# Kernel tuning notes

Measured on AMD Instinct MI355X. Metric: run time of the kernel, lower is better.

## Reference

```python
import jax, jax.numpy as jnp
import numpy as np

D_MODEL = 256
NUM_HEADS = 8
DEPTH = D_MODEL // NUM_HEADS
NEG_BIG = -1e9


def setup_inputs() -> dict:
    key = jax.random.key(0)
    ks = jax.random.split(key, 8)
    B, S = 4, 2048
    inp = {
        "v": jax.random.normal(ks[0], (B, S, D_MODEL), dtype=jnp.float32),
        "k": jax.random.normal(ks[1], (B, S, D_MODEL), dtype=jnp.float32),
        "q": jax.random.normal(ks[2], (B, S, D_MODEL), dtype=jnp.float32),
        "mask": jnp.ones((B, S), dtype=jnp.float32),
        # kernel_size-1 Conv1D without bias == dense projection (d_in, d_out)
        "Wq": jax.random.normal(ks[3], (D_MODEL, D_MODEL), dtype=jnp.float32) * 0.05,
        "Wk": jax.random.normal(ks[4], (D_MODEL, D_MODEL), dtype=jnp.float32) * 0.05,
        "Wv": jax.random.normal(ks[5], (D_MODEL, D_MODEL), dtype=jnp.float32) * 0.05,
        "Wo": jax.random.normal(ks[6], (D_MODEL, D_MODEL), dtype=jnp.float32) * 0.05,
    }
    return inp


def _split_heads(x):
    # (B, S, d_model) -> (B, H, S, depth)
    B, S, _ = x.shape
    return x.reshape(B, S, NUM_HEADS, DEPTH).transpose(0, 2, 1, 3)


def reference(v, k, q, mask, Wq, Wk, Wv, Wo):
    B, S, _ = q.shape
    qh = _split_heads(q @ Wq)  # (B,H,Sq,depth)
    kh = _split_heads(k @ Wk)  # (B,H,Sk,depth)
    vh = _split_heads(v @ Wv)  # (B,H,Sk,depth)

    scale = 1.0 / jnp.sqrt(jnp.asarray(DEPTH, dtype=jnp.float32))
    logits = jnp.einsum("bhqd,bhkd->bhqk", qh, kh) * scale  # (B,H,Sq,Sk)
    mask_att = mask[:, None, None, :]  # broadcast over heads and query dim
    logits = logits + (1.0 - mask_att) * NEG_BIG
    attn = jax.nn.softmax(logits, axis=-1)  # (B,H,Sq,Sk)

    ctx = jnp.einsum("bhqk,bhkd->bhqd", attn, vh)  # (B,H,Sq,depth)
    concat = ctx.transpose(0, 2, 1, 3).reshape(B, S, D_MODEL)
    out = concat @ Wo
    return (out, attn)
```

## Files before the change

### kernel.cpp

```cpp
#include <hip/hip_runtime.h>

#define BB 4
#define HH 8
#define SS 2048
#define DD 32
#define DMODEL 256
#define NEG_BIG_F (-1000000000.0f)
#define SCALE 0.17677669529663687f
#define L2E 1.4426950408889634f
#define SC2 (SCALE * L2E)

typedef short short8 __attribute__((ext_vector_type(8)));
typedef float float4_ __attribute__((ext_vector_type(4)));

__device__ __forceinline__ unsigned short f2bf(float x) {
  unsigned u = __float_as_uint(x);
  u += 0x7FFFu + ((u >> 16) & 1u);
  return (unsigned short)(u >> 16);
}

__device__ __forceinline__ unsigned cvtpk(float lo, float hi) {
  unsigned u;
  asm("v_cvt_pk_bf16_f32 %0, %1, %2" : "=v"(u) : "v"(lo), "v"(hi));
  return u;
}

__global__ __launch_bounds__(256) void prep_w(
    const float* __restrict__ Wq, const float* __restrict__ Wk,
    const float* __restrict__ Wv, const float* __restrict__ Wo,
    unsigned short* __restrict__ wt) {
  __shared__ float tile[32][33];
  int z = blockIdx.z;
  const float* W = (z == 0) ? Wq : (z == 1) ? Wk : (z == 2) ? Wv : Wo;
  unsigned short* dst = wt + (size_t)z * DMODEL * DMODEL;
  int k0 = blockIdx.x * 32, n0 = blockIdx.y * 32;
  int tx = threadIdx.x & 31, ty = threadIdx.x >> 5;
  for (int r = ty; r < 32; r += 8)
    tile[r][tx] = W[(size_t)(k0 + r) * DMODEL + n0 + tx];
  __syncthreads();
  for (int r = ty; r < 32; r += 8)
    dst[(size_t)(n0 + r) * DMODEL + k0 + tx] = f2bf(tile[tx][r]);
}

__global__ __launch_bounds__(256) void proj_kernel(
    const float* __restrict__ q, const float* __restrict__ k,
    const float* __restrict__ v, const unsigned short* __restrict__ wt,
    unsigned short* __restrict__ qh, unsigned short* __restrict__ kh,
    unsigned short* __restrict__ vT) {
  int z = blockIdx.z;
  const float* src = (z == 0) ? q : (z == 1) ? k : v;
  const unsigned short* Wt = wt + (size_t)z * DMODEL * DMODEL;

  int w = threadIdx.x >> 6, lane = threadIdx.x & 63, l16 = lane & 15,
      g = lane >> 4;
  int row = blockIdx.x * 64 + w * 16 + l16;
  int n0 = blockIdx.y * 64;

  float4_ z4 = {0.f, 0.f, 0.f, 0.f};
  float4_ acc[4] = {z4, z4, z4, z4};

  for (int k0 = 0; k0 < DMODEL; k0 += 32) {
    const float4_* ap = (const float4_*)(src + (size_t)row * DMODEL + k0 + 8 * g);
    float4_ a0 = ap[0], a1 = ap[1];
    short8 a;
#pragma unroll
    for (int j = 0; j < 4; ++j) {
      a[j] = (short)f2bf(a0[j]);
      a[4 + j] = (short)f2bf(a1[j]);
    }
#pragma unroll
    for (int cb = 0; cb < 4; ++cb) {
      int n = n0 + cb * 16 + l16;
      short8 bfr = *(const short8*)(Wt + (size_t)n * DMODEL + k0 + 8 * g);
      acc[cb] = __builtin_amdgcn_mfma_f32_16x16x32_bf16(a, bfr, acc[cb], 0, 0, 0);
    }
  }

  int rowbase = blockIdx.x * 64 + w * 16 + 4 * g;
#pragma unroll
  for (int cb = 0; cb < 4; ++cb) {
#pragma unroll
    for (int rr = 0; rr < 4; ++rr) {
      int r = rowbase + rr;
      int c = n0 + cb * 16 + l16;
      int b = r >> 11, s = r & (SS - 1);
      int h = c >> 5, d = c & 31;
      int bh = b * HH + h;
      unsigned short val = f2bf(acc[cb][rr]);
      if (z == 2) {
        vT[((size_t)bh * DD + d) * SS + s] = val;
      } else {
        unsigned short* dst = (z == 0) ? qh : kh;
        dst[((size_t)bh * SS + s) * DD + d] = val;
      }
    }
  }
}

__global__ __launch_bounds__(256) void fused_attn(
    const unsigned short* __restrict__ qh, const unsigned short* __restrict__ kh,
    const unsigned short* __restrict__ vT, const float* __restrict__ mask,
    float* __restrict__ attn_out, unsigned short* __restrict__ concat) {
  __shared__ float biasl2[SS];
  __shared__ unsigned short at[4][16][72];

  int bh = blockIdx.y;
  int b = bh >> 3, h = bh & 7;
  for (int i = threadIdx.x; i < SS; i += 256)
    biasl2[i] = (1.0f - mask[(size_t)b * SS + i]) * (NEG_BIG_F * L2E);
  __syncthreads();

  int w = threadIdx.x >> 6, lane = threadIdx.x & 63, l16 = lane & 15,
      g = lane >> 4;
  int q0 = blockIdx.x * 64 + w * 16;

  short8 qa = *(const short8*)(qh + ((size_t)bh * SS + q0 + l16) * DD + 8 * g);

  const unsigned short* kbase = kh + (size_t)bh * SS * DD;
  const unsigned short* vtb = vT + (size_t)bh * DD * SS;
  float4_ z4 = {0.f, 0.f, 0.f, 0.f};

  float l = 0.f;
#pragma unroll 4
  for (int t = 0; t < 128; ++t) {
    short8 kf = *(const short8*)(kbase + (size_t)(t * 16 + l16) * DD + 8 * g);
    float4_ r = __builtin_amdgcn_mfma_f32_16x16x32_bf16(kf, qa, z4, 0, 0, 0);
    float4_ b4 = *(const float4_*)&biasl2[t * 16 + 4 * g];
    float e0 = exp2f(fmaf(r[0], SC2, b4[0]));
    float e1 = exp2f(fmaf(r[1], SC2, b4[1]));
    float e2 = exp2f(fmaf(r[2], SC2, b4[2]));
    float e3 = exp2f(fmaf(r[3], SC2, b4[3]));
    l += (e0 + e1) + (e2 + e3);
  }
#pragma unroll
  for (int off = 16; off < 64; off <<= 1) l += __shfl_xor(l, off);
  float dq = log2f(l);

  float* arow = attn_out + (size_t)bh * SS * SS + (size_t)(q0 + l16) * SS;
  float4_ acc0 = z4, acc1 = z4;

  for (int kb = 0; kb < SS; kb += 64) {
#pragma unroll
    for (int ks = 0; ks < 2; ++ks) {
#pragma unroll
      for (int kt = 0; kt < 2; ++kt) {
        int k0 = kb + ks * 32 + kt * 16;
        int col = ks * 32 + kt * 16 + 4 * g;
        short8 kf = *(const short8*)(kbase + (size_t)(k0 + l16) * DD + 8 * g);
        float4_ r = __builtin_amdgcn_mfma_f32_16x16x32_bf16(kf, qa, z4, 0, 0, 0);
        float4_ b4 = *(const float4_*)&biasl2[kb + col];
        float4_ p;
#pragma unroll
        for (int rr = 0; rr < 4; ++rr)
          p[rr] = exp2f(fmaf(r[rr], SC2, b4[rr] - dq));
        *(float4_*)(arow + kb + col) = p;
        uint2 pk;
        pk.x = cvtpk(p[0], p[1]);
        pk.y = cvtpk(p[2], p[3]);
        *(uint2*)&at[w][l16][col] = pk;
      }
      short8 pa = *(const short8*)&at[w][l16][ks * 32 + 8 * g];
      short8 b0 =
          *(const short8*)(vtb + (size_t)l16 * SS + kb + ks * 32 + 8 * g);
      short8 b1 =
          *(const short8*)(vtb + (size_t)(16 + l16) * SS + kb + ks * 32 + 8 * g);
      acc0 = __builtin_amdgcn_mfma_f32_16x16x32_bf16(pa, b0, acc0, 0, 0, 0);
      acc1 = __builtin_amdgcn_mfma_f32_16x16x32_bf16(pa, b1, acc1, 0, 0, 0);
    }
  }

#pragma unroll
  for (int rr = 0; rr < 4; ++rr) {
    int s = q0 + 4 * g + rr;
    size_t base = ((size_t)b * SS + s) * DMODEL + h * DD;
    concat[base + l16] = f2bf(acc0[rr]);
    concat[base + 16 + l16] = f2bf(acc1[rr]);
  }
}

__global__ __launch_bounds__(256) void outgemm_kernel(
    const unsigned short* __restrict__ concat,
    const unsigned short* __restrict__ wot,
    float* __restrict__ out) {
  int w = threadIdx.x >> 6, lane = threadIdx.x & 63, l16 = lane & 15,
      g = lane >> 4;
  int row = blockIdx.x * 64 + w * 16 + l16;
  int n0 = blockIdx.y * 64;
  float4_ z4 = {0.f, 0.f, 0.f, 0.f};
  float4_ acc[4] = {z4, z4, z4, z4};
  for (int k0 = 0; k0 < DMODEL; k0 += 32) {
    short8 a = *(const short8*)(concat + (size_t)row * DMODEL + k0 + 8 * g);
#pragma unroll
    for (int cb = 0; cb < 4; ++cb) {
      int n = n0 + cb * 16 + l16;
      short8 bfr = *(const short8*)(wot + (size_t)n * DMODEL + k0 + 8 * g);
      acc[cb] = __builtin_amdgcn_mfma_f32_16x16x32_bf16(a, bfr, acc[cb], 0, 0, 0);
    }
  }
  int rowbase = blockIdx.x * 64 + w * 16 + 4 * g;
#pragma unroll
  for (int cb = 0; cb < 4; ++cb)
#pragma unroll
    for (int rr = 0; rr < 4; ++rr)
      out[(size_t)(rowbase + rr) * DMODEL + n0 + cb * 16 + l16] = acc[cb][rr];
}

extern "C" void kernel_launch(void* const* d_in, const int* in_sizes, int n_in,
                              void* d_out, int out_size, void* d_ws,
                              size_t ws_size, hipStream_t stream) {
  const float* v = (const float*)d_in[0];
  const float* k = (const float*)d_in[1];
  const float* q = (const float*)d_in[2];
  const float* mask = (const float*)d_in[3];
  const float* Wq = (const float*)d_in[4];
  const float* Wk = (const float*)d_in[5];
  const float* Wv = (const float*)d_in[6];
  const float* Wo = (const float*)d_in[7];

  float* out = (float*)d_out;
  float* attn = out + (size_t)BB * SS * DMODEL;

  const size_t NH = (size_t)BB * HH * SS * DD;
  unsigned short* qh = (unsigned short*)d_ws;
  unsigned short* kh = qh + NH;
  unsigned short* vT = kh + NH;
  unsigned short* concat = vT + NH;
  unsigned short* wt = concat + (size_t)BB * SS * DMODEL;

  prep_w<<<dim3(8, 8, 4), 256, 0, stream>>>(Wq, Wk, Wv, Wo, wt);
  proj_kernel<<<dim3(128, 4, 3), 256, 0, stream>>>(q, k, v, wt, qh, kh, vT);
  fused_attn<<<dim3(32, 32), 256, 0, stream>>>(qh, kh, vT, mask, attn, concat);
  outgemm_kernel<<<dim3(128, 4), 256, 0, stream>>>(
      concat, wt + (size_t)3 * DMODEL * DMODEL, out);
}
```

Baseline: 267.5 us.

## Stage attention probabilities in LDS for row-contiguous stores; precompute bias and transpose V

The attention kernel now writes fp32 probabilities for a 128-key chunk into per-wave LDS. Each lane then stores 32 contiguous floats of the attn row, replacing the scattered float4 stores taken straight from the MFMA layout. The mask bias moves to a separate global kernel, and V is written row-major and then transposed by a dedicated tiled kernel instead of strided scattered stores. This adds two small launches and an extra V round trip through memory, in exchange for better write coalescing on the large attn output.

```diff
diff --git a/kernel.cpp b/kernel.cpp
--- a/kernel.cpp
+++ b/kernel.cpp
@@ -12,6 +12,7 @@
 
 typedef short short8 __attribute__((ext_vector_type(8)));
 typedef float float4_ __attribute__((ext_vector_type(4)));
+typedef unsigned int uint4_ __attribute__((ext_vector_type(4)));
 
 __device__ __forceinline__ unsigned short f2bf(float x) {
   unsigned u = __float_as_uint(x);
@@ -42,14 +43,21 @@
     dst[(size_t)(n0 + r) * DMODEL + k0 + tx] = f2bf(tile[tx][r]);
 }
 
+__global__ __launch_bounds__(256) void biask(const float* __restrict__ mask,
+                                             float* __restrict__ biasg) {
+  int i = blockIdx.x * 256 + threadIdx.x;
+  if (i < BB * SS) biasg[i] = (1.0f - mask[i]) * (NEG_BIG_F * L2E);
+}
+
 __global__ __launch_bounds__(256) void proj_kernel(
     const float* __restrict__ q, const float* __restrict__ k,
     const float* __restrict__ v, const unsigned short* __restrict__ wt,
     unsigned short* __restrict__ qh, unsigned short* __restrict__ kh,
-    unsigned short* __restrict__ vT) {
+    unsigned short* __restrict__ vh) {
   int z = blockIdx.z;
   const float* src = (z == 0) ? q : (z == 1) ? k : v;
   const unsigned short* Wt = wt + (size_t)z * DMODEL * DMODEL;
+  unsigned short* dst = (z == 0) ? qh : (z == 1) ? kh : vh;
 
   int w = threadIdx.x >> 6, lane = threadIdx.x & 63, l16 = lane & 15,
       g = lane >> 4;
@@ -86,30 +94,36 @@
       int b = r >> 11, s = r & (SS - 1);
       int h = c >> 5, d = c & 31;
       int bh = b * HH + h;
-      unsigned short val = f2bf(acc[cb][rr]);
-      if (z == 2) {
-        vT[((size_t)bh * DD + d) * SS + s] = val;
-      } else {
-        unsigned short* dst = (z == 0) ? qh : kh;
-        dst[((size_t)bh * SS + s) * DD + d] = val;
-      }
-    }
+      dst[((size_t)bh * SS + s) * DD + d] = f2bf(acc[cb][rr]);
+    }
+  }
+}
+
+__global__ __launch_bounds__(256) void transpose_v(
+    const unsigned short* __restrict__ vh, unsigned short* __restrict__ vT) {
+  __shared__ unsigned short tile[32][66];
+  int bh = blockIdx.y;
+  int s0 = blockIdx.x * 64;
+  int t = threadIdx.x;
+  for (int i = t; i < 64 * 32; i += 256) {
+    int s = i >> 5, d = i & 31;
+    tile[d][s] = vh[((size_t)bh * SS + s0 + s) * DD + d];
+  }
+  __syncthreads();
+  for (int i = t; i < 32 * 64; i += 256) {
+    int d = i >> 6, s = i & 63;
+    vT[((size_t)bh * DD + d) * SS + s0 + s] = tile[d][s];
   }
 }
 
 __global__ __launch_bounds__(256) void fused_attn(
     const unsigned short* __restrict__ qh, const unsigned short* __restrict__ kh,
-    const unsigned short* __restrict__ vT, const float* __restrict__ mask,
+    const unsigned short* __restrict__ vT, const float* __restrict__ biasg,
     float* __restrict__ attn_out, unsigned short* __restrict__ concat) {
-  __shared__ float biasl2[SS];
-  __shared__ unsigned short at[4][16][72];
+  __shared__ float pf[4][16][132];
 
   int bh = blockIdx.y;
   int b = bh >> 3, h = bh & 7;
-  for (int i = threadIdx.x; i < SS; i += 256)
-    biasl2[i] = (1.0f - mask[(size_t)b * SS + i]) * (NEG_BIG_F * L2E);
-  __syncthreads();
-
   int w = threadIdx.x >> 6, lane = threadIdx.x & 63, l16 = lane & 15,
       g = lane >> 4;
   int q0 = blockIdx.x * 64 + w * 16;
@@ -118,6 +132,7 @@
 
   const unsigned short* kbase = kh + (size_t)bh * SS * DD;
   const unsigned short* vtb = vT + (size_t)bh * DD * SS;
+  const float* bias = biasg + (size_t)b * SS;
   float4_ z4 = {0.f, 0.f, 0.f, 0.f};
 
   float l = 0.f;
@@ -125,7 +140,7 @@
   for (int t = 0; t < 128; ++t) {
     short8 kf = *(const short8*)(kbase + (size_t)(t * 16 + l16) * DD + 8 * g);
     float4_ r = __builtin_amdgcn_mfma_f32_16x16x32_bf16(kf, qa, z4, 0, 0, 0);
-    float4_ b4 = *(const float4_*)&biasl2[t * 16 + 4 * g];
+    float4_ b4 = *(const float4_*)(bias + t * 16 + 4 * g);
     float e0 = exp2f(fmaf(r[0], SC2, b4[0]));
     float e1 = exp2f(fmaf(r[1], SC2, b4[1]));
     float e2 = exp2f(fmaf(r[2], SC2, b4[2]));
@@ -139,33 +154,48 @@
   float* arow = attn_out + (size_t)bh * SS * SS + (size_t)(q0 + l16) * SS;
   float4_ acc0 = z4, acc1 = z4;
 
-  for (int kb = 0; kb < SS; kb += 64) {
-#pragma unroll
-    for (int ks = 0; ks < 2; ++ks) {
-#pragma unroll
-      for (int kt = 0; kt < 2; ++kt) {
-        int k0 = kb + ks * 32 + kt * 16;
-        int col = ks * 32 + kt * 16 + 4 * g;
-        short8 kf = *(const short8*)(kbase + (size_t)(k0 + l16) * DD + 8 * g);
-        float4_ r = __builtin_amdgcn_mfma_f32_16x16x32_bf16(kf, qa, z4, 0, 0, 0);
-        float4_ b4 = *(const float4_*)&biasl2[kb + col];
-        float4_ p;
-#pragma unroll
-        for (int rr = 0; rr < 4; ++rr)
-          p[rr] = exp2f(fmaf(r[rr], SC2, b4[rr] - dq));
-        *(float4_*)(arow + kb + col) = p;
-        uint2 pk;
-        pk.x = cvtpk(p[0], p[1]);
-        pk.y = cvtpk(p[2], p[3]);
-        *(uint2*)&at[w][l16][col] = pk;
+  for (int C = 0; C < SS; C += 128) {
+#pragma unroll
+    for (int sub = 0; sub < 2; ++sub) {
+      int kb = C + sub * 64;
+#pragma unroll
+      for (int ks = 0; ks < 2; ++ks) {
+#pragma unroll
+        for (int kt = 0; kt < 2; ++kt) {
+          int k0 = kb + ks * 32 + kt * 16;
+          short8 kf =
+              *(const short8*)(kbase + (size_t)(k0 + l16) * DD + 8 * g);
+          float4_ r =
+              __builtin_amdgcn_mfma_f32_16x16x32_bf16(kf, qa, z4, 0, 0, 0);
+          float4_ b4 = *(const float4_*)(bias + k0 + 4 * g);
+          float4_ p;
+#pragma unroll
+          for (int rr = 0; rr < 4; ++rr)
+            p[rr] = exp2f(fmaf(r[rr], SC2, b4[rr] - dq));
+          *(float4_*)&pf[w][l16][sub * 64 + ks * 32 + kt * 16 + 4 * g] = p;
+        }
+        float4_ f0 = *(float4_*)&pf[w][l16][sub * 64 + ks * 32 + 8 * g];
+        float4_ f1 = *(float4_*)&pf[w][l16][sub * 64 + ks * 32 + 8 * g + 4];
+        uint4_ pw;
+        pw[0] = cvtpk(f0[0], f0[1]);
+        pw[1] = cvtpk(f0[2], f0[3]);
+        pw[2] = cvtpk(f1[0], f1[1]);
+        pw[3] = cvtpk(f1[2], f1[3]);
+        short8 pa = *(short8*)&pw;
+        short8 b0 =
+            *(const short8*)(vtb + (size_t)l16 * SS + kb + ks * 32 + 8 * g);
+        short8 b1 = *(const short8*)(vtb + (size_t)(16 + l16) * SS + kb +
+                                     ks * 32 + 8 * g);
+        acc0 = __builtin_amdgcn_mfma_f32_16x16x32_bf16(pa, b0, acc0, 0, 0, 0);
+        acc1 = __builtin_amdgcn_mfma_f32_16x16x32_bf16(pa, b1, acc1, 0, 0, 0);
       }
-      short8 pa = *(const short8*)&at[w][l16][ks * 32 + 8 * g];
-      short8 b0 =
-          *(const short8*)(vtb + (size_t)l16 * SS + kb + ks * 32 + 8 * g);
-      short8 b1 =
-          *(const short8*)(vtb + (size_t)(16 + l16) * SS + kb + ks * 32 + 8 * g);
-      acc0 = __builtin_amdgcn_mfma_f32_16x16x32_bf16(pa, b0, acc0, 0, 0, 0);
-      acc1 = __builtin_amdgcn_mfma_f32_16x16x32_bf16(pa, b1, acc1, 0, 0, 0);
+    }
+    asm volatile("s_waitcnt lgkmcnt(0)");
+    __builtin_amdgcn_sched_barrier(0);
+#pragma unroll
+    for (int j = 0; j < 8; ++j) {
+      float4_ vdr = *(float4_*)&pf[w][l16][32 * g + 4 * j];
+      *(float4_*)(arow + C + 32 * g + 4 * j) = vdr;
     }
   }
 
@@ -223,13 +253,17 @@
   const size_t NH = (size_t)BB * HH * SS * DD;
   unsigned short* qh = (unsigned short*)d_ws;
   unsigned short* kh = qh + NH;
-  unsigned short* vT = kh + NH;
+  unsigned short* vh = kh + NH;
+  unsigned short* vT = vh + NH;
   unsigned short* concat = vT + NH;
   unsigned short* wt = concat + (size_t)BB * SS * DMODEL;
+  float* biasg = (float*)(wt + (size_t)4 * DMODEL * DMODEL);
 
   prep_w<<<dim3(8, 8, 4), 256, 0, stream>>>(Wq, Wk, Wv, Wo, wt);
-  proj_kernel<<<dim3(128, 4, 3), 256, 0, stream>>>(q, k, v, wt, qh, kh, vT);
-  fused_attn<<<dim3(32, 32), 256, 0, stream>>>(qh, kh, vT, mask, attn, concat);
+  biask<<<dim3(32), 256, 0, stream>>>(mask, biasg);
+  proj_kernel<<<dim3(128, 4, 3), 256, 0, stream>>>(q, k, v, wt, qh, kh, vh);
+  transpose_v<<<dim3(32, 32), 256, 0, stream>>>(vh, vT);
+  fused_attn<<<dim3(32, 32), 256, 0, stream>>>(qh, kh, vT, biasg, attn, concat);
   outgemm_kernel<<<dim3(128, 4), 256, 0, stream>>>(
       concat, wt + (size_t)3 * DMODEL * DMODEL, out);
 }
```

Result: slower. 359.3 us (+34.3%).
